# Performance work log

Hardware: AMD Instinct MI355X
Metric: run time of the kernel (lower is better)

Reference implementation:

```python
import jax, jax.numpy as jnp
import numpy as np

NT = 32          # nt_states
T = 64           # t_states
ST = NT + T      # total states
NEG = -1e9       # matches self.huge fill


def setup_inputs() -> dict:
    key = jax.random.key(0)
    k1, k2, k3 = jax.random.split(key, 3)
    B, n = 8, 28
    return {
        "unary_scores": jax.random.normal(k1, (B, n, T), dtype=jnp.float32),
        "rule_scores": jax.random.normal(k2, (B, NT, ST, ST), dtype=jnp.float32),
        "root_scores": jax.random.normal(k3, (B, NT), dtype=jnp.float32),
    }


def _inside(unary_scores, rule_scores, root_scores):
    # Chart indexed beta[b, width, start, state]; span (s, s+w) lives at [b, w, s].
    # Invalid (state-range) slots hold NEG, so exp() underflows them to exactly 0,
    # reproducing the terminal/nonterminal slice logic of the torch code.
    B, n, _ = unary_scores.shape
    beta = jnp.full((B, n, n, ST), NEG, dtype=unary_scores.dtype)
    beta = beta.at[:, 0, :, NT:].set(unary_scores)  # width-0 diagonal: preterminals

    mrule = rule_scores.max(axis=(2, 3))                    # [B, A]
    erule = jnp.exp(rule_scores - mrule[:, :, None, None])  # [B, A, L, R]

    for w in range(1, n):
        S = n - w                     # number of valid start positions
        k = np.arange(w)              # split offset: u = s + k
        # left child: span (s, s+k) -> width k, start s
        left = beta[:, :w, :S, :]                                  # [B, w, S, ST]
        # right child: span (s+k+1, s+w) -> width w-1-k, start s+k+1
        sr = k[:, None] + 1 + np.arange(S)[None, :]                # [w, S]
        right = beta[:, (w - 1 - k)[:, None], sr, :]               # [B, w, S, ST]

        # stable logsumexp over (k, l, r) via exp-space matmuls
        ml = left.max(-1)                                          # [B, w, S]
        mr = right.max(-1)                                         # [B, w, S]
        M = (ml + mr).max(1)                                       # [B, S]
        el = jnp.exp(left - ml[..., None])
        er = jnp.exp(right - mr[..., None] + (ml + mr - M[:, None, :])[..., None])
        numer = jnp.einsum('bksl,bksr->bslr', el, er)              # [B, S, L, R]
        total = jnp.einsum('bslr,balr->bsa', numer, erule)         # [B, S, A]
        score = jnp.log(total) + M[..., None] + mrule[:, None, :]
        beta = beta.at[:, w, :S, :NT].set(score)

    top = beta[:, n - 1, 0, :NT] + root_scores                     # span (0, n-1)
    return jax.nn.logsumexp(top, axis=1)                           # log Z, [B]


def reference(unary_scores, rule_scores, root_scores):
    return _inside(unary_scores, rule_scores, root_scores)
```

## Files before the change

kernel.cpp:

```cpp
#include <hip/hip_runtime.h>
#include <cstdint>
#include <cstddef>


#define NMAX 28
#define SLOT 17344
#define MROW 17280
#define MPROW 17312

#define O_BW1 0
#define O_BMX 960
#define O_G   1744
#define O_MSP 2528
#define O_EMR 2560
#define O_NUM 2592
#define O_RED 6160
#define O_ELT 20496
#define O_ELK 6160
#define O_ERK 14480
#define O_TRI 22800
#define LDSF  34864

__device__ __forceinline__ int off32(int w, int n) {
    return (w - 1) * n - (w * (w - 1)) / 2;
}
__device__ __forceinline__ float gload(const float* p) {
    return __hip_atomic_load(p, __ATOMIC_RELAXED, __HIP_MEMORY_SCOPE_AGENT);
}
__device__ __forceinline__ void gstore(float* p, float v) {
    __hip_atomic_store(p, v, __ATOMIC_RELAXED, __HIP_MEMORY_SCOPE_AGENT);
}
__device__ __forceinline__ unsigned gloadu(const unsigned* p) {
    return __hip_atomic_load(p, __ATOMIC_RELAXED, __HIP_MEMORY_SCOPE_AGENT);
}
__device__ __forceinline__ void gstoreu(unsigned* p, unsigned v) {
    __hip_atomic_store(p, v, __ATOMIC_RELAXED, __HIP_MEMORY_SCOPE_AGENT);
}
__device__ __forceinline__ float dot4acc(float4 m, float4 t, float acc) {
    return fmaf(m.x, t.x, fmaf(m.y, t.y, fmaf(m.z, t.z, fmaf(m.w, t.w, acc))));
}

__global__ __launch_bounds__(256) void mrule_kernel(const float* __restrict__ rule,
                                                    float* __restrict__ mrule,
                                                    unsigned* __restrict__ flags) {
    int a = blockIdx.x, b = blockIdx.y, tid = threadIdx.x;
    if (a == 0 && tid < 32)
        gstoreu(&flags[b * 32 + tid], (tid >= 16 && tid < 20) ? 2u : 0u);
    const float* base = rule + (size_t)(b * 32 + a) * 9216;
    float v = -3.0e38f;
    for (int i = tid; i < 9216; i += 256) v = fmaxf(v, base[i]);
    for (int off = 32; off > 0; off >>= 1) v = fmaxf(v, __shfl_xor(v, off, 64));
    __shared__ float red[4];
    if ((tid & 63) == 0) red[tid >> 6] = v;
    __syncthreads();
    if (tid == 0)
        mrule[b * 32 + a] = fmaxf(fmaxf(red[0], red[1]), fmaxf(red[2], red[3]));
}

__global__ __launch_bounds__(256) void pack_kernel(const float* __restrict__ rule,
                                                   const float* __restrict__ mrule,
                                                   float* __restrict__ E_TT,
                                                   float* __restrict__ E_TN,
                                                   float* __restrict__ E_NT,
                                                   float* __restrict__ E_NN) {
    int b = blockIdx.y, tid = threadIdx.x;
    int a = tid & 31;
    int cc = blockIdx.x * 8 + (tid >> 5);
    float mr = mrule[b * 32 + a];
    int l, r;
    float* dst;
    if (cc < 1024) {
        int flat = cc * 4;
        l = 32 + (flat >> 6); r = 32 + (flat & 63);
        dst = E_TT + ((size_t)(b * 1024 + cc) * 32 + a) * 4;
    } else if (cc < 1536) {
        int flat = (cc - 1024) * 4;
        l = 32 + (flat >> 5); r = flat & 31;
        dst = E_TN + ((size_t)(b * 512 + (cc - 1024)) * 32 + a) * 4;
    } else if (cc < 2048) {
        int flat = (cc - 1536) * 4;
        l = flat >> 6; r = 32 + (flat & 63);
        dst = E_NT + ((size_t)(b * 512 + (cc - 1536)) * 32 + a) * 4;
    } else {
        int flat = (cc - 2048) * 4;
        l = flat >> 5; r = flat & 31;
        dst = E_NN + ((size_t)(b * 256 + (cc - 2048)) * 32 + a) * 4;
    }
    const float4 v = *(const float4*)(rule + (((size_t)(b * 32 + a) * 96 + l) * 96 + r));
    float4 o;
    o.x = expf(v.x - mr); o.y = expf(v.y - mr);
    o.z = expf(v.z - mr); o.w = expf(v.w - mr);
    *(float4*)dst = o;
}

__device__ __forceinline__ void spin_flags(const unsigned* f, unsigned tgt, int tid) {
    if (tid < 64) {
        for (;;) {
            unsigned v = (tid < 20) ? gloadu(&f[tid]) : tgt;
            if (__ballot(v < tgt) == 0ull) break;
            __builtin_amdgcn_s_sleep(2);
        }
    }
    __syncthreads();
}

__global__ __launch_bounds__(1024, 4) void inside_kernel(
    const float* __restrict__ unary, const float* __restrict__ mrule,
    const float* __restrict__ E_TT, const float* __restrict__ E_TN,
    const float* __restrict__ E_NT, const float* __restrict__ E_NN,
    float* __restrict__ part, const float* __restrict__ root,
    float* __restrict__ out, unsigned* __restrict__ flags, int n) {
    extern __shared__ float lds[];
    const int b = blockIdx.x / 20, ch = blockIdx.x % 20;
    const int tid = threadIdx.x;
    const int a = tid & 31;
    unsigned* const myflags = flags + b * 32;
    float* const pbase = part + (size_t)(b * 4) * SLOT;

    float4 e4[2];
    {
        const float4* Eq;
        int base4;
        if (ch < 16) { Eq = (const float4*)E_TT + (size_t)b * 32768; base4 = ch * 64; }
        else         { Eq = (const float4*)E_NN + (size_t)b * 8192;  base4 = (ch - 16) * 64; }
        #pragma unroll
        for (int i = 0; i < 2; ++i)
            e4[i] = Eq[(size_t)(base4 + (tid >> 5) * 2 + i) * 32 + a];
    }
    if (tid < 32) lds[O_EMR + tid] = __expf(mrule[b * 32 + tid]);
    for (int pos = tid >> 6; pos < n; pos += 16) {
        int t = tid & 63;
        float v = unary[((size_t)b * n + pos) * 64 + t];
        float m = v;
        for (int off = 32; off > 0; off >>= 1) m = fmaxf(m, __shfl_xor(m, off, 64));
        if (t == 0) lds[O_BMX + pos] = m;
        if (ch < 16) lds[O_ELT + t * 29 + pos] = __expf(v - m);
    }
    __syncthreads();

    if (ch < 16) {
        for (int w = 1; w < n; ++w) {
            const int S = n - w;
            float* pbW = pbase + (size_t)(w & 3) * SLOT;

            if (w >= 2) {
                spin_flags(myflags, (unsigned)(w - 1), tid);
                const int wp = w - 1;
                const float* pbP = pbase + (size_t)(wp & 3) * SLOT;
                if (tid < (S + 1) * 32) {
                    int s = tid >> 5, aa = tid & 31;
                    float q[20];
                    #pragma unroll
                    for (int c = 0; c < 20; ++c) q[c] = gload(&pbP[c * 864 + tid]);
                    float tT = (((q[0] + q[1]) + (q[2] + q[3])) + ((q[4] + q[5]) + (q[6] + q[7])))
                             + (((q[8] + q[9]) + (q[10] + q[11])) + ((q[12] + q[13]) + (q[14] + q[15])));
                    float t = tT;
                    if (wp >= 3) {
                        float tN = (q[16] + q[17]) + (q[18] + q[19]);
                        float Mp = gload(&pbP[MPROW + s]);
                        t = fmaf(__expf(Mp - lds[O_MSP + s]), tN, tT);
                    }
                    float t2 = t * lds[O_EMR + aa];
                    float m2 = t2;
                    for (int off = 16; off > 0; off >>= 1)
                        m2 = fmaxf(m2, __shfl_xor(m2, off, 32));
                    lds[O_BW1 + aa * 30 + s] = t2 / m2;
                    if (aa == 0)
                        lds[O_BMX + wp * NMAX + s] = __logf(m2) + lds[O_MSP + s];
                }
                __syncthreads();
            }

            if (tid < S) {
                int s = tid;
                float M = -3.0e38f;
                for (int k = 0; k < w; ++k)
                    M = fmaxf(M, lds[O_BMX + k * NMAX + s] +
                                  lds[O_BMX + (w - 1 - k) * NMAX + s + k + 1]);
                lds[O_MSP + s] = M;
                lds[O_G + s] =
                    __expf(lds[O_BMX + s] + lds[O_BMX + (w - 1) * NMAX + s + 1] - M);
                lds[O_G + NMAX + s] =
                    __expf(lds[O_BMX + (w - 1) * NMAX + s] + lds[O_BMX + s + w] - M);
                if (ch == 0) gstore(&pbW[MROW + s], M);
            }
            __syncthreads();

            {
                const int cL = tid & 255, sh = tid >> 8;
                const bool tn = (w >= 2) && (ch < 8);
                const int cc = (w == 1) ? ch * 256 + cL
                             : (ch < 8 ? ch * 256 + cL : (ch - 8) * 256 + cL);
                int l, r;
                if (tn) { l = cc >> 5; r = cc & 31; }
                else    { l = cc >> 6; r = cc & 63; }
                unsigned short* np = (unsigned short*)(lds + O_NUM);
                for (int s = sh; s < S; s += 4) {
                    float v;
                    if (w == 1)
                        v = lds[O_ELT + l * 29 + s] * lds[O_ELT + r * 29 + (s + 1)] *
                            lds[O_G + s];
                    else if (tn)
                        v = lds[O_ELT + l * 29 + s] * lds[O_BW1 + r * 30 + (s + 1)] *
                            lds[O_G + s];
                    else
                        v = lds[O_BW1 + l * 30 + s] * lds[O_ELT + r * 29 + (s + w)] *
                            lds[O_G + NMAX + s];
                    unsigned u = __float_as_uint(v);
                    np[s * 264 + cL] = (unsigned short)((u + 0x7fffu + ((u >> 16) & 1u)) >> 16);
                }
            }
            __syncthreads();

            {
                const char* nbase = (const char*)(lds + O_NUM);
                const int g32 = tid >> 5, wv = tid >> 6;
                const bool lowhalf = (tid & 32) == 0;
                for (int s = 0; s < S; ++s) {
                    uint4 u = *(const uint4*)(nbase + s * 528 + g32 * 16);
                    float acc = 0.f;
                    #define LO(q) __uint_as_float((q) << 16)
                    #define HI(q) __uint_as_float((q) & 0xffff0000u)
                    acc = fmaf(LO(u.x), e4[0].x, acc); acc = fmaf(HI(u.x), e4[0].y, acc);
                    acc = fmaf(LO(u.y), e4[0].z, acc); acc = fmaf(HI(u.y), e4[0].w, acc);
                    acc = fmaf(LO(u.z), e4[1].x, acc); acc = fmaf(HI(u.z), e4[1].y, acc);
                    acc = fmaf(LO(u.w), e4[1].z, acc); acc = fmaf(HI(u.w), e4[1].w, acc);
                    #undef LO
                    #undef HI
                    acc += __shfl_xor(acc, 32, 64);
                    if (lowhalf) lds[O_RED + wv * 896 + s * 32 + a] = acc;
                }
            }
            __syncthreads();

            if (tid < S * 32) {
                float t = 0.f;
                #pragma unroll
                for (int g2 = 0; g2 < 16; ++g2) t += lds[O_RED + g2 * 896 + tid];
                gstore(&pbW[ch * 864 + tid], t);
            }
            __syncthreads();
            if (tid == 0) gstoreu(&myflags[ch], (unsigned)w);

            if (w == 1) {
                const float4* Eq = (ch < 8)
                    ? (const float4*)E_TN + (size_t)b * 16384 + (size_t)(ch * 64) * 32
                    : (const float4*)E_NT + (size_t)b * 16384 + (size_t)((ch - 8) * 64) * 32;
                #pragma unroll
                for (int i = 0; i < 2; ++i)
                    e4[i] = Eq[(size_t)((tid >> 5) * 2 + i) * 32 + a];
            }
        }

        if (ch == 0) {
            spin_flags(myflags, (unsigned)(n - 1), tid);
            if (tid < 32) {
                const float* pbP = pbase + (size_t)((n - 1) & 3) * SLOT;
                float q[20];
                #pragma unroll
                for (int c = 0; c < 20; ++c) q[c] = gload(&pbP[c * 864 + tid]);
                float tT = (((q[0] + q[1]) + (q[2] + q[3])) + ((q[4] + q[5]) + (q[6] + q[7])))
                         + (((q[8] + q[9]) + (q[10] + q[11])) + ((q[12] + q[13]) + (q[14] + q[15])));
                float tN = (q[16] + q[17]) + (q[18] + q[19]);
                float Mp = gload(&pbP[MPROW + 0]);
                float t = fmaf(__expf(Mp - lds[O_MSP + 0]), tN, tT);
                float v = __logf(t) + lds[O_MSP + 0] + mrule[b * 32 + tid] + root[b * 32 + tid];
                float m = v;
                for (int off = 16; off > 0; off >>= 1) m = fmaxf(m, __shfl_xor(m, off, 32));
                float e = __expf(v - m);
                for (int off = 16; off > 0; off >>= 1) e += __shfl_xor(e, off, 32);
                if (tid == 0) out[b] = m + __logf(e);
            }
        }
    } else {
        for (int w = 3; w < n; ++w) {
            const int S = n - w, Sp2 = S | 1;
            int q4 = (w - 2 + 3) >> 2; if (!(q4 & 1)) ++q4;
            const int K4 = 4 * q4;
            float* pbW = pbase + (size_t)(w & 3) * SLOT;

            spin_flags(myflags, (unsigned)(w - 2), tid);

            {
                const int wf = w - 2;
                const float* pbF = pbase + (size_t)(wf & 3) * SLOT;
                if (tid < (n - wf) * 32) {
                    int s = tid >> 5, aa = tid & 31;
                    float q[20];
                    #pragma unroll
                    for (int c = 0; c < 20; ++c) q[c] = gload(&pbF[c * 864 + tid]);
                    float tT = (((q[0] + q[1]) + (q[2] + q[3])) + ((q[4] + q[5]) + (q[6] + q[7])))
                             + (((q[8] + q[9]) + (q[10] + q[11])) + ((q[12] + q[13]) + (q[14] + q[15])));
                    float Mf = gload(&pbF[MROW + s]);
                    float t = tT;
                    if (wf >= 3) {
                        float tN = (q[16] + q[17]) + (q[18] + q[19]);
                        float Mp = gload(&pbF[MPROW + s]);
                        t = fmaf(__expf(Mp - Mf), tN, tT);
                    }
                    float t2 = t * lds[O_EMR + aa];
                    float m2 = t2;
                    for (int off = 16; off > 0; off >>= 1)
                        m2 = fmaxf(m2, __shfl_xor(m2, off, 32));
                    lds[O_TRI + (off32(wf, n) + s) * 32 + aa] = t2 / m2;
                    if (aa == 0) lds[O_BMX + wf * NMAX + s] = __logf(m2) + Mf;
                }
                __syncthreads();
            }

            if (tid < (w - 2) * 32) {
                int k = (tid >> 5) + 1, s = tid & 31;
                if (s < S) {
                    float Mp = -3.0e38f;
                    for (int k2 = 1; k2 <= w - 2; ++k2)
                        Mp = fmaxf(Mp, lds[O_BMX + k2 * NMAX + s] +
                                       lds[O_BMX + (w - 1 - k2) * NMAX + s + k2 + 1]);
                    lds[O_G + k * NMAX + s] =
                        __expf(lds[O_BMX + k * NMAX + s] +
                               lds[O_BMX + (w - 1 - k) * NMAX + s + k + 1] - Mp);
                    if (k == 1 && ch == 16) gstore(&pbW[MPROW + s], Mp);
                }
            }
            __syncthreads();

            if (tid < S * 32) {
                int s = tid >> 5, sym = tid & 31;
                int off = (sym * Sp2 + s) * K4;
                for (int kk = 1; kk <= w - 2; ++kk) {
                    lds[O_ELK + off + kk - 1] =
                        lds[O_TRI + (off32(kk, n) + s) * 32 + sym];
                    lds[O_ERK + off + kk - 1] =
                        lds[O_TRI + (off32(w - 1 - kk, n) + s + kk + 1) * 32 + sym] *
                        lds[O_G + kk * NMAX + s];
                }
                for (int k = w - 2; k < K4; ++k) {
                    lds[O_ELK + off + k] = 0.f;
                    lds[O_ERK + off + k] = 0.f;
                }
            }
            __syncthreads();

            {
                const int cL = tid & 255, sh = tid >> 8;
                const int cc = (ch - 16) * 256 + cL;
                const int l = cc >> 5, r = cc & 31;
                unsigned short* np = (unsigned short*)(lds + O_NUM);
                for (int s = sh; s < S; s += 4) {
                    const float* elp = lds + O_ELK + (l * Sp2 + s) * K4;
                    const float* erp = lds + O_ERK + (r * Sp2 + s) * K4;
                    float acc = 0.f;
                    for (int j = 0; j < K4; j += 4)
                        acc = dot4acc(*(const float4*)(elp + j),
                                      *(const float4*)(erp + j), acc);
                    unsigned u = __float_as_uint(acc);
                    np[s * 264 + cL] = (unsigned short)((u + 0x7fffu + ((u >> 16) & 1u)) >> 16);
                }
            }
            __syncthreads();

            {
                const char* nbase = (const char*)(lds + O_NUM);
                const int g32 = tid >> 5, wv = tid >> 6;
                const bool lowhalf = (tid & 32) == 0;
                for (int s = 0; s < S; ++s) {
                    uint4 u = *(const uint4*)(nbase + s * 528 + g32 * 16);
                    float acc = 0.f;
                    #define LO(q) __uint_as_float((q) << 16)
                    #define HI(q) __uint_as_float((q) & 0xffff0000u)
                    acc = fmaf(LO(u.x), e4[0].x, acc); acc = fmaf(HI(u.x), e4[0].y, acc);
                    acc = fmaf(LO(u.y), e4[0].z, acc); acc = fmaf(HI(u.y), e4[0].w, acc);
                    acc = fmaf(LO(u.z), e4[1].x, acc); acc = fmaf(HI(u.z), e4[1].y, acc);
                    acc = fmaf(LO(u.w), e4[1].z, acc); acc = fmaf(HI(u.w), e4[1].w, acc);
                    #undef LO
                    #undef HI
                    acc += __shfl_xor(acc, 32, 64);
                    if (lowhalf) lds[O_RED + wv * 896 + s * 32 + a] = acc;
                }
            }
            __syncthreads();

            if (tid < S * 32) {
                float t = 0.f;
                #pragma unroll
                for (int g2 = 0; g2 < 16; ++g2) t += lds[O_RED + g2 * 896 + tid];
                gstore(&pbW[ch * 864 + tid], t);
            }
            __syncthreads();
            if (tid == 0) gstoreu(&myflags[ch], (unsigned)w);
        }
    }
}

extern "C" void kernel_launch(void* const* d_in, const int* in_sizes, int n_in,
                              void* d_out, int out_size, void* d_ws, size_t ws_size,
                              hipStream_t stream) {
    const float* unary = (const float*)d_in[0];
    const float* rule  = (const float*)d_in[1];
    const float* root  = (const float*)d_in[2];
    float* out = (float*)d_out;

    const int B = in_sizes[2] / 32;
    int n = in_sizes[0] / (B * 64);

    float* ws = (float*)d_ws;
    float* mrule  = ws;
    float* E_TT   = mrule + (size_t)B * 32;
    float* E_TN   = E_TT + (size_t)B * 131072;
    float* E_NT   = E_TN + (size_t)B * 65536;
    float* E_NN   = E_NT + (size_t)B * 65536;
    float* part   = E_NN + (size_t)B * 32768;
    unsigned* flags = (unsigned*)(part + (size_t)B * 4 * SLOT);

    mrule_kernel<<<dim3(32, B), 256, 0, stream>>>(rule, mrule, flags);
    pack_kernel<<<dim3(288, B), 256, 0, stream>>>(rule, mrule, E_TT, E_TN, E_NT, E_NN);

    hipFuncSetAttribute((const void*)inside_kernel,
                        hipFuncAttributeMaxDynamicSharedMemorySize, LDSF * 4);

    void* args[] = {
        (void*)&unary, (void*)&mrule,
        (void*)&E_TT, (void*)&E_TN, (void*)&E_NT, (void*)&E_NN,
        (void*)&part, (void*)&root, (void*)&out, (void*)&flags, (void*)&n
    };
    hipLaunchCooperativeKernel((void*)inside_kernel, dim3(B * 20), dim3(1024),
                               args, LDSF * 4, stream);
}
```

Baseline: 242.7 us.

## Precontract terminal rule tensors with unary scores to shrink the inside recursion

```diff
diff --git a/kernel.cpp b/kernel.cpp
--- a/kernel.cpp
+++ b/kernel.cpp
@@ -4,22 +4,22 @@
 
 
 #define NMAX 28
-#define SLOT 17344
-#define MROW 17280
-#define MPROW 17312
-
-#define O_BW1 0
-#define O_BMX 960
-#define O_G   1744
-#define O_MSP 2528
-#define O_EMR 2560
-#define O_NUM 2592
-#define O_RED 6160
-#define O_ELT 20496
-#define O_ELK 6160
-#define O_ERK 14480
-#define O_TRI 22800
-#define LDSF  34864
+#define SLOTF 10368
+#define T_ELT 0
+#define T_BW1 1856
+#define T_BMX 2816
+#define T_MSP 3600
+#define T_GG  3632
+#define T_HB  3712
+#define T_FB  10880
+#define N_BMX 0
+#define N_GP  784
+#define N_NUM 1568
+#define N_RED 5132
+#define N_ELK 5132
+#define N_ERK 13452
+#define N_TRI 21772
+#define LDSF  33836
 
 __device__ __forceinline__ int off32(int w, int n) {
     return (w - 1) * n - (w * (w - 1)) / 2;
@@ -39,185 +39,306 @@
 __device__ __forceinline__ float dot4acc(float4 m, float4 t, float acc) {
     return fmaf(m.x, t.x, fmaf(m.y, t.y, fmaf(m.z, t.z, fmaf(m.w, t.w, acc))));
 }
-
-__global__ __launch_bounds__(256) void mrule_kernel(const float* __restrict__ rule,
-                                                    float* __restrict__ mrule,
-                                                    unsigned* __restrict__ flags) {
-    int a = blockIdx.x, b = blockIdx.y, tid = threadIdx.x;
-    if (a == 0 && tid < 32)
-        gstoreu(&flags[b * 32 + tid], (tid >= 16 && tid < 20) ? 2u : 0u);
-    const float* base = rule + (size_t)(b * 32 + a) * 9216;
-    float v = -3.0e38f;
-    for (int i = tid; i < 9216; i += 256) v = fmaxf(v, base[i]);
-    for (int off = 32; off > 0; off >>= 1) v = fmaxf(v, __shfl_xor(v, off, 64));
-    __shared__ float red[4];
-    if ((tid & 63) == 0) red[tid >> 6] = v;
-    __syncthreads();
-    if (tid == 0)
-        mrule[b * 32 + a] = fmaxf(fmaxf(red[0], red[1]), fmaxf(red[2], red[3]));
-}
-
-__global__ __launch_bounds__(256) void pack_kernel(const float* __restrict__ rule,
-                                                   const float* __restrict__ mrule,
-                                                   float* __restrict__ E_TT,
-                                                   float* __restrict__ E_TN,
-                                                   float* __restrict__ E_NT,
-                                                   float* __restrict__ E_NN) {
-    int b = blockIdx.y, tid = threadIdx.x;
-    int a = tid & 31;
-    int cc = blockIdx.x * 8 + (tid >> 5);
-    float mr = mrule[b * 32 + a];
-    int l, r;
-    float* dst;
-    if (cc < 1024) {
-        int flat = cc * 4;
-        l = 32 + (flat >> 6); r = 32 + (flat & 63);
-        dst = E_TT + ((size_t)(b * 1024 + cc) * 32 + a) * 4;
-    } else if (cc < 1536) {
-        int flat = (cc - 1024) * 4;
-        l = 32 + (flat >> 5); r = flat & 31;
-        dst = E_TN + ((size_t)(b * 512 + (cc - 1024)) * 32 + a) * 4;
-    } else if (cc < 2048) {
-        int flat = (cc - 1536) * 4;
-        l = flat >> 6; r = 32 + (flat & 63);
-        dst = E_NT + ((size_t)(b * 512 + (cc - 1536)) * 32 + a) * 4;
-    } else {
-        int flat = (cc - 2048) * 4;
-        l = flat >> 5; r = flat & 31;
-        dst = E_NN + ((size_t)(b * 256 + (cc - 2048)) * 32 + a) * 4;
-    }
-    const float4 v = *(const float4*)(rule + (((size_t)(b * 32 + a) * 96 + l) * 96 + r));
-    float4 o;
-    o.x = expf(v.x - mr); o.y = expf(v.y - mr);
-    o.z = expf(v.z - mr); o.w = expf(v.w - mr);
-    *(float4*)dst = o;
-}
-
-__device__ __forceinline__ void spin_flags(const unsigned* f, unsigned tgt, int tid) {
+__device__ __forceinline__ float maxM(const float* bmx, int w, int s) {
+    float M = -3.0e38f;
+    for (int k = 0; k < w; ++k)
+        M = fmaxf(M, bmx[k * NMAX + s] + bmx[(w - 1 - k) * NMAX + s + k + 1]);
+    return M;
+}
+__device__ __forceinline__ float maxMp(const float* bmx, int w, int s) {
+    float M = -3.0e38f;
+    for (int k = 1; k <= w - 2; ++k)
+        M = fmaxf(M, bmx[k * NMAX + s] + bmx[(w - 1 - k) * NMAX + s + k + 1]);
+    return M;
+}
+__device__ __forceinline__ float finalize_sum(const float* pp, bool hasNN,
+                                              float Mp, float Mw) {
+    float x[12];
+    #pragma unroll
+    for (int c = 0; c < 12; ++c) x[c] = gload(pp + c);
+    float tT = (((x[0] + x[1]) + (x[2] + x[3])) + ((x[4] + x[5]) + (x[6] + x[7])));
+    float t = tT;
+    if (hasNN) {
+        float tN = (x[8] + x[9]) + (x[10] + x[11]);
+        t = fmaf(__expf(Mp - Mw), tN, tT);
+    }
+    return t;
+}
+__device__ __forceinline__ void spin12(const unsigned* f, unsigned tgt, int tid) {
     if (tid < 64) {
         for (;;) {
-            unsigned v = (tid < 20) ? gloadu(&f[tid]) : tgt;
+            unsigned v = (tid < 12) ? gloadu(&f[tid]) : tgt;
             if (__ballot(v < tgt) == 0ull) break;
-            __builtin_amdgcn_s_sleep(2);
+            __builtin_amdgcn_s_sleep(1);
         }
     }
     __syncthreads();
 }
 
-__global__ __launch_bounds__(1024, 4) void inside_kernel(
-    const float* __restrict__ unary, const float* __restrict__ mrule,
-    const float* __restrict__ E_TT, const float* __restrict__ E_TN,
-    const float* __restrict__ E_NT, const float* __restrict__ E_NN,
+__global__ __launch_bounds__(256) void prep_kernel(const float* __restrict__ unary,
+                                                   float* __restrict__ elT_g,
+                                                   float* __restrict__ bmax0_g,
+                                                   unsigned* __restrict__ flags, int n) {
+    int b = blockIdx.x, tid = threadIdx.x;
+    if (tid < 12) gstoreu(&flags[b * 32 + tid], (tid >= 8) ? 2u : 0u);
+    for (int pos = tid >> 6; pos < n; pos += 4) {
+        int t = tid & 63;
+        float v = unary[((size_t)(b * n) + pos) * 64 + t];
+        float m = v;
+        for (int off = 32; off > 0; off >>= 1) m = fmaxf(m, __shfl_xor(m, off, 64));
+        elT_g[(size_t)b * 64 * n + t * n + pos] = __expf(v - m);
+        if (t == 0) bmax0_g[b * 32 + pos] = m;
+    }
+}
+
+__global__ __launch_bounds__(256) void pack_kernel(const float* __restrict__ rule,
+                                                   const float* __restrict__ elT_g,
+                                                   float* __restrict__ H_g,
+                                                   float* __restrict__ F_g,
+                                                   float* __restrict__ G_g,
+                                                   float* __restrict__ E_NN, int n) {
+    extern __shared__ float sl[];
+    int b = blockIdx.y, aa = blockIdx.x, tid = threadIdx.x;
+    const float4* rs4 = (const float4*)(rule + (size_t)(b * 32 + aa) * 9216);
+    for (int i = tid; i < 2304; i += 256) {
+        float4 v = rs4[i];
+        float4 o;
+        o.x = __expf(v.x); o.y = __expf(v.y); o.z = __expf(v.z); o.w = __expf(v.w);
+        ((float4*)sl)[i] = o;
+    }
+    for (int i = tid; i < 64 * n; i += 256)
+        sl[9216 + i] = elT_g[(size_t)b * 64 * n + i];
+    __syncthreads();
+    const float* elt = sl + 9216;
+    {
+        int c4 = tid;
+        if (c4 < 256) {
+            int flat = c4 * 4, l = flat >> 5, r = flat & 31;
+            float4 o = *(const float4*)(sl + l * 96 + r);
+            *(float4*)(E_NN + ((size_t)(b * 256 + c4) * 32 + aa) * 4) = o;
+        }
+    }
+    for (int i = tid; i < 64 * n; i += 256) {
+        int r = i / n, s = i - r * n;
+        float acc = 0.f;
+        for (int l = 0; l < 64; ++l)
+            acc = fmaf(elt[l * n + s], sl[(32 + l) * 96 + 32 + r], acc);
+        H_g[((size_t)(b * 64 + r) * n + s) * 32 + aa] = acc;
+    }
+    for (int i = tid; i < 32 * n; i += 256) {
+        int r = i / n, s = i - r * n;
+        float acc = 0.f;
+        for (int l = 0; l < 64; ++l)
+            acc = fmaf(elt[l * n + s], sl[(32 + l) * 96 + r], acc);
+        F_g[((size_t)(b * 32 + r) * n + s) * 32 + aa] = acc;
+    }
+    for (int i = tid; i < 32 * n; i += 256) {
+        int l = i / n, s = i - l * n;
+        float acc = 0.f;
+        for (int r = 0; r < 64; ++r)
+            acc = fmaf(elt[r * n + s], sl[l * 96 + 32 + r], acc);
+        G_g[((size_t)(b * 32 + l) * n + s) * 32 + aa] = acc;
+    }
+}
+
+__global__ __launch_bounds__(1024, 1) void inside_kernel(
+    const float* __restrict__ elT_g, const float* __restrict__ bmax0_g,
+    const float* __restrict__ H_g, const float* __restrict__ F_g,
+    const float* __restrict__ G_g, const float* __restrict__ E_NN,
     float* __restrict__ part, const float* __restrict__ root,
     float* __restrict__ out, unsigned* __restrict__ flags, int n) {
     extern __shared__ float lds[];
-    const int b = blockIdx.x / 20, ch = blockIdx.x % 20;
+    const int b = blockIdx.x / 12, ch = blockIdx.x % 12;
     const int tid = threadIdx.x;
     const int a = tid & 31;
     unsigned* const myflags = flags + b * 32;
-    float* const pbase = part + (size_t)(b * 4) * SLOT;
-
-    float4 e4[2];
-    {
-        const float4* Eq;
-        int base4;
-        if (ch < 16) { Eq = (const float4*)E_TT + (size_t)b * 32768; base4 = ch * 64; }
-        else         { Eq = (const float4*)E_NN + (size_t)b * 8192;  base4 = (ch - 16) * 64; }
-        #pragma unroll
-        for (int i = 0; i < 2; ++i)
-            e4[i] = Eq[(size_t)(base4 + (tid >> 5) * 2 + i) * 32 + a];
-    }
-    if (tid < 32) lds[O_EMR + tid] = __expf(mrule[b * 32 + tid]);
-    for (int pos = tid >> 6; pos < n; pos += 16) {
-        int t = tid & 63;
-        float v = unary[((size_t)b * n + pos) * 64 + t];
-        float m = v;
-        for (int off = 32; off > 0; off >>= 1) m = fmaxf(m, __shfl_xor(m, off, 64));
-        if (t == 0) lds[O_BMX + pos] = m;
-        if (ch < 16) lds[O_ELT + t * 29 + pos] = __expf(v - m);
-    }
-    __syncthreads();
-
-    if (ch < 16) {
+    float* const pbase = part + (size_t)(b * 4) * SLOTF;
+
+    if (ch < 8) {
+        for (int i = tid; i < 64 * n; i += 1024) {
+            int t = i / n, pos = i - t * n;
+            lds[T_ELT + t * 29 + pos] = elT_g[(size_t)b * 64 * n + i];
+        }
+        for (int i = tid; i < 8 * n * 32; i += 1024)
+            lds[T_HB + i] = H_g[(size_t)(b * 64 + ch * 8) * n * 32 + i];
+        {
+            const float* src = (ch < 4)
+                ? F_g + (size_t)(b * 32 + ch * 8) * n * 32
+                : G_g + (size_t)(b * 32 + (ch - 4) * 8) * n * 32;
+            for (int i = tid; i < 8 * n * 32; i += 1024) lds[T_FB + i] = src[i];
+        }
+        if (tid < n) lds[T_BMX + tid] = bmax0_g[b * 32 + tid];
+        __syncthreads();
+
         for (int w = 1; w < n; ++w) {
             const int S = n - w;
-            float* pbW = pbase + (size_t)(w & 3) * SLOT;
+            float* pbW = pbase + (size_t)(w & 3) * SLOTF;
 
             if (w >= 2) {
-                spin_flags(myflags, (unsigned)(w - 1), tid);
+                spin12(myflags, (unsigned)(w - 1), tid);
                 const int wp = w - 1;
-                const float* pbP = pbase + (size_t)(wp & 3) * SLOT;
+                const bool hasNN = (wp >= 3);
+                const float* pbP = pbase + (size_t)(wp & 3) * SLOTF;
                 if (tid < (S + 1) * 32) {
                     int s = tid >> 5, aa = tid & 31;
-                    float q[20];
-                    #pragma unroll
-                    for (int c = 0; c < 20; ++c) q[c] = gload(&pbP[c * 864 + tid]);
-                    float tT = (((q[0] + q[1]) + (q[2] + q[3])) + ((q[4] + q[5]) + (q[6] + q[7])))
-                             + (((q[8] + q[9]) + (q[10] + q[11])) + ((q[12] + q[13]) + (q[14] + q[15])));
-                    float t = tT;
-                    if (wp >= 3) {
-                        float tN = (q[16] + q[17]) + (q[18] + q[19]);
-                        float Mp = gload(&pbP[MPROW + s]);
-                        t = fmaf(__expf(Mp - lds[O_MSP + s]), tN, tT);
-                    }
-                    float t2 = t * lds[O_EMR + aa];
-                    float m2 = t2;
+                    float Mp = maxMp(lds + T_BMX, wp, s);
+                    float t = finalize_sum(pbP + (size_t)tid * 12, hasNN,
+                                           Mp, lds[T_MSP + s]);
+                    float m2 = t;
                     for (int off = 16; off > 0; off >>= 1)
                         m2 = fmaxf(m2, __shfl_xor(m2, off, 32));
-                    lds[O_BW1 + aa * 30 + s] = t2 / m2;
+                    lds[T_BW1 + aa * 30 + s] = t / m2;
                     if (aa == 0)
-                        lds[O_BMX + wp * NMAX + s] = __logf(m2) + lds[O_MSP + s];
+                        lds[T_BMX + wp * NMAX + s] = __logf(m2) + lds[T_MSP + s];
                 }
                 __syncthreads();
             }
 
             if (tid < S) {
                 int s = tid;
-                float M = -3.0e38f;
-                for (int k = 0; k < w; ++k)
-                    M = fmaxf(M, lds[O_BMX + k * NMAX + s] +
-                                  lds[O_BMX + (w - 1 - k) * NMAX + s + k + 1]);
-                lds[O_MSP + s] = M;
-                lds[O_G + s] =
-                    __expf(lds[O_BMX + s] + lds[O_BMX + (w - 1) * NMAX + s + 1] - M);
-                lds[O_G + NMAX + s] =
-                    __expf(lds[O_BMX + (w - 1) * NMAX + s] + lds[O_BMX + s + w] - M);
-                if (ch == 0) gstore(&pbW[MROW + s], M);
+                float M = maxM(lds + T_BMX, w, s);
+                lds[T_MSP + s] = M;
+                lds[T_GG + s] =
+                    __expf(lds[T_BMX + s] + lds[T_BMX + (w - 1) * NMAX + s + 1] - M);
+                lds[T_GG + 32 + s] =
+                    __expf(lds[T_BMX + (w - 1) * NMAX + s] + lds[T_BMX + s + w] - M);
+            }
+            __syncthreads();
+
+            if (tid < S * 32) {
+                int s = tid >> 5;
+                float acc = 0.f;
+                if (w == 1) {
+                    #pragma unroll
+                    for (int j = 0; j < 8; ++j)
+                        acc = fmaf(lds[T_ELT + (ch * 8 + j) * 29 + (s + 1)],
+                                   lds[T_HB + (j * n + s) * 32 + a], acc);
+                } else if (ch < 4) {
+                    #pragma unroll
+                    for (int j = 0; j < 8; ++j)
+                        acc = fmaf(lds[T_BW1 + (ch * 8 + j) * 30 + (s + 1)],
+                                   lds[T_FB + (j * n + s) * 32 + a], acc);
+                    acc *= lds[T_GG + s];
+                } else {
+                    #pragma unroll
+                    for (int j = 0; j < 8; ++j)
+                        acc = fmaf(lds[T_BW1 + ((ch - 4) * 8 + j) * 30 + s],
+                                   lds[T_FB + (j * n + (s + w)) * 32 + a], acc);
+                    acc *= lds[T_GG + 32 + s];
+                }
+                gstore(&pbW[(size_t)tid * 12 + ch], acc);
+            }
+            __syncthreads();
+            if (tid == 0) gstoreu(&myflags[ch], (unsigned)w);
+        }
+
+        if (ch == 0) {
+            spin12(myflags, (unsigned)(n - 1), tid);
+            if (tid < 32) {
+                const int wp = n - 1;
+                const float* pbP = pbase + (size_t)(wp & 3) * SLOTF;
+                float Mp = maxMp(lds + T_BMX, wp, 0);
+                float t = finalize_sum(pbP + (size_t)tid * 12, true,
+                                       Mp, lds[T_MSP + 0]);
+                float v = __logf(t) + lds[T_MSP + 0] + root[b * 32 + tid];
+                float m = v;
+                for (int off = 16; off > 0; off >>= 1)
+                    m = fmaxf(m, __shfl_xor(m, off, 32));
+                float e = __expf(v - m);
+                for (int off = 16; off > 0; off >>= 1) e += __shfl_xor(e, off, 32);
+                if (tid == 0) out[b] = m + __logf(e);
+            }
+        }
+    } else {
+        float4 e4[2];
+        {
+            const float4* Eq = (const float4*)E_NN + (size_t)b * 8192;
+            int base = (ch - 8) * 64 + (tid >> 5) * 2;
+            e4[0] = Eq[(size_t)base * 32 + a];
+            e4[1] = Eq[(size_t)(base + 1) * 32 + a];
+        }
+        if (tid < n) lds[N_BMX + tid] = bmax0_g[b * 32 + tid];
+        __syncthreads();
+
+        for (int w = 3; w < n; ++w) {
+            const int S = n - w, Sp2 = S | 1;
+            int q4 = (w - 2 + 3) >> 2; if (!(q4 & 1)) ++q4;
+            const int K4 = 4 * q4;
+            float* pbW = pbase + (size_t)(w & 3) * SLOTF;
+
+            spin12(myflags, (unsigned)(w - 2), tid);
+
+            {
+                const int wf = w - 2;
+                const bool hasNN = (wf >= 3);
+                const float* pbF_ = pbase + (size_t)(wf & 3) * SLOTF;
+                if (tid < (n - wf) * 32) {
+                    int s = tid >> 5, aa = tid & 31;
+                    float Mw = maxM(lds + N_BMX, wf, s);
+                    float Mp = maxMp(lds + N_BMX, wf, s);
+                    float t = finalize_sum(pbF_ + (size_t)tid * 12, hasNN, Mp, Mw);
+                    float m2 = t;
+                    for (int off = 16; off > 0; off >>= 1)
+                        m2 = fmaxf(m2, __shfl_xor(m2, off, 32));
+                    lds[N_TRI + (off32(wf, n) + s) * 32 + aa] = t / m2;
+                    if (aa == 0) lds[N_BMX + wf * NMAX + s] = __logf(m2) + Mw;
+                }
+                __syncthreads();
+            }
+
+            if (tid < (w - 2) * 32) {
+                int k = (tid >> 5) + 1, s = tid & 31;
+                if (s < S) {
+                    float Mp = maxMp(lds + N_BMX, w, s);
+                    lds[N_GP + k * NMAX + s] =
+                        __expf(lds[N_BMX + k * NMAX + s] +
+                               lds[N_BMX + (w - 1 - k) * NMAX + s + k + 1] - Mp);
+                }
+            }
+            __syncthreads();
+
+            if (tid < S * 32) {
+                int s = tid >> 5, sym = tid & 31;
+                int off = (sym * Sp2 + s) * K4;
+                for (int kk = 1; kk <= w - 2; ++kk) {
+                    lds[N_ELK + off + kk - 1] =
+                        lds[N_TRI + (off32(kk, n) + s) * 32 + sym];
+                    lds[N_ERK + off + kk - 1] =
+                        lds[N_TRI + (off32(w - 1 - kk, n) + s + kk + 1) * 32 + sym] *
+                        lds[N_GP + kk * NMAX + s];
+                }
+                for (int k = w - 2; k < K4; ++k) {
+                    lds[N_ELK + off + k] = 0.f;
+                    lds[N_ERK + off + k] = 0.f;
+                }
             }
             __syncthreads();
 
             {
                 const int cL = tid & 255, sh = tid >> 8;
-                const bool tn = (w >= 2) && (ch < 8);
-                const int cc = (w == 1) ? ch * 256 + cL
-                             : (ch < 8 ? ch * 256 + cL : (ch - 8) * 256 + cL);
-                int l, r;
-                if (tn) { l = cc >> 5; r = cc & 31; }
-                else    { l = cc >> 6; r = cc & 63; }
-                unsigned short* np = (unsigned short*)(lds + O_NUM);
+                const int cc = (ch - 8) * 256 + cL;
+                const int l = cc >> 5, r = cc & 31;
+                unsigned short* np = (unsigned short*)(lds + N_NUM);
                 for (int s = sh; s < S; s += 4) {
-                    float v;
-                    if (w == 1)
-                        v = lds[O_ELT + l * 29 + s] * lds[O_ELT + r * 29 + (s + 1)] *
-                            lds[O_G + s];
-                    else if (tn)
-                        v = lds[O_ELT + l * 29 + s] * lds[O_BW1 + r * 30 + (s + 1)] *
-                            lds[O_G + s];
-                    else
-                        v = lds[O_BW1 + l * 30 + s] * lds[O_ELT + r * 29 + (s + w)] *
-                            lds[O_G + NMAX + s];
-                    unsigned u = __float_as_uint(v);
-                    np[s * 264 + cL] = (unsigned short)((u + 0x7fffu + ((u >> 16) & 1u)) >> 16);
+                    const float* elp = lds + N_ELK + (l * Sp2 + s) * K4;
+                    const float* erp = lds + N_ERK + (r * Sp2 + s) * K4;
+                    float acc = 0.f;
+                    for (int j = 0; j < K4; j += 4)
+                        acc = dot4acc(*(const float4*)(elp + j),
+                                      *(const float4*)(erp + j), acc);
+                    unsigned u = __float_as_uint(acc);
+                    np[s * 264 + cL] =
+                        (unsigned short)((u + 0x7fffu + ((u >> 16) & 1u)) >> 16);
                 }
             }
             __syncthreads();
 
             {
-                const char* nbase = (const char*)(lds + O_NUM);
-                const int g32 = tid >> 5, wv = tid >> 6;
-                const bool lowhalf = (tid & 32) == 0;
+                const char* nb = (const char*)(lds + N_NUM);
+                const int g = tid >> 5, wv = tid >> 6;
+                const bool low = (tid & 32) == 0;
                 for (int s = 0; s < S; ++s) {
-                    uint4 u = *(const uint4*)(nbase + s * 528 + g32 * 16);
+                    uint4 u = *(const uint4*)(nb + s * 528 + g * 16);
                     float acc = 0.f;
                     #define LO(q) __uint_as_float((q) << 16)
                     #define HI(q) __uint_as_float((q) & 0xffff0000u)
@@ -228,7 +349,7 @@
                     #undef LO
                     #undef HI
                     acc += __shfl_xor(acc, 32, 64);
-                    if (lowhalf) lds[O_RED + wv * 896 + s * 32 + a] = acc;
+                    if (low) lds[N_RED + wv * 896 + s * 32 + a] = acc;
                 }
             }
             __syncthreads();
@@ -236,154 +357,8 @@
             if (tid < S * 32) {
                 float t = 0.f;
                 #pragma unroll
-                for (int g2 = 0; g2 < 16; ++g2) t += lds[O_RED + g2 * 896 + tid];
-                gstore(&pbW[ch * 864 + tid], t);
-            }
-            __syncthreads();
-            if (tid == 0) gstoreu(&myflags[ch], (unsigned)w);
-
-            if (w == 1) {
-                const float4* Eq = (ch < 8)
-                    ? (const float4*)E_TN + (size_t)b * 16384 + (size_t)(ch * 64) * 32
-                    : (const float4*)E_NT + (size_t)b * 16384 + (size_t)((ch - 8) * 64) * 32;
-                #pragma unroll
-                for (int i = 0; i < 2; ++i)
-                    e4[i] = Eq[(size_t)((tid >> 5) * 2 + i) * 32 + a];
-            }
-        }
-
-        if (ch == 0) {
-            spin_flags(myflags, (unsigned)(n - 1), tid);
-            if (tid < 32) {
-                const float* pbP = pbase + (size_t)((n - 1) & 3) * SLOT;
-                float q[20];
-                #pragma unroll
-                for (int c = 0; c < 20; ++c) q[c] = gload(&pbP[c * 864 + tid]);
-                float tT = (((q[0] + q[1]) + (q[2] + q[3])) + ((q[4] + q[5]) + (q[6] + q[7])))
-                         + (((q[8] + q[9]) + (q[10] + q[11])) + ((q[12] + q[13]) + (q[14] + q[15])));
-                float tN = (q[16] + q[17]) + (q[18] + q[19]);
-                float Mp = gload(&pbP[MPROW + 0]);
-                float t = fmaf(__expf(Mp - lds[O_MSP + 0]), tN, tT);
-                float v = __logf(t) + lds[O_MSP + 0] + mrule[b * 32 + tid] + root[b * 32 + tid];
-                float m = v;
-                for (int off = 16; off > 0; off >>= 1) m = fmaxf(m, __shfl_xor(m, off, 32));
-                float e = __expf(v - m);
-                for (int off = 16; off > 0; off >>= 1) e += __shfl_xor(e, off, 32);
-                if (tid == 0) out[b] = m + __logf(e);
-            }
-        }
-    } else {
-        for (int w = 3; w < n; ++w) {
-            const int S = n - w, Sp2 = S | 1;
-            int q4 = (w - 2 + 3) >> 2; if (!(q4 & 1)) ++q4;
-            const int K4 = 4 * q4;
-            float* pbW = pbase + (size_t)(w & 3) * SLOT;
-
-            spin_flags(myflags, (unsigned)(w - 2), tid);
-
-            {
-                const int wf = w - 2;
-                const float* pbF = pbase + (size_t)(wf & 3) * SLOT;
-                if (tid < (n - wf) * 32) {
-                    int s = tid >> 5, aa = tid & 31;
-                    float q[20];
-                    #pragma unroll
-                    for (int c = 0; c < 20; ++c) q[c] = gload(&pbF[c * 864 + tid]);
-                    float tT = (((q[0] + q[1]) + (q[2] + q[3])) + ((q[4] + q[5]) + (q[6] + q[7])))
-                             + (((q[8] + q[9]) + (q[10] + q[11])) + ((q[12] + q[13]) + (q[14] + q[15])));
-                    float Mf = gload(&pbF[MROW + s]);
-                    float t = tT;
-                    if (wf >= 3) {
-                        float tN = (q[16] + q[17]) + (q[18] + q[19]);
-                        float Mp = gload(&pbF[MPROW + s]);
-                        t = fmaf(__expf(Mp - Mf), tN, tT);
-                    }
-                    float t2 = t * lds[O_EMR + aa];
-                    float m2 = t2;
-                    for (int off = 16; off > 0; off >>= 1)
-                        m2 = fmaxf(m2, __shfl_xor(m2, off, 32));
-                    lds[O_TRI + (off32(wf, n) + s) * 32 + aa] = t2 / m2;
-                    if (aa == 0) lds[O_BMX + wf * NMAX + s] = __logf(m2) + Mf;
-                }
-                __syncthreads();
-            }
-
-            if (tid < (w - 2) * 32) {
-                int k = (tid >> 5) + 1, s = tid & 31;
-                if (s < S) {
-                    float Mp = -3.0e38f;
-                    for (int k2 = 1; k2 <= w - 2; ++k2)
-                        Mp = fmaxf(Mp, lds[O_BMX + k2 * NMAX + s] +
-                                       lds[O_BMX + (w - 1 - k2) * NMAX + s + k2 + 1]);
-                    lds[O_G + k * NMAX + s] =
-                        __expf(lds[O_BMX + k * NMAX + s] +
-                               lds[O_BMX + (w - 1 - k) * NMAX + s + k + 1] - Mp);
-                    if (k == 1 && ch == 16) gstore(&pbW[MPROW + s], Mp);
-                }
-            }
-            __syncthreads();
-
-            if (tid < S * 32) {
-                int s = tid >> 5, sym = tid & 31;
-                int off = (sym * Sp2 + s) * K4;
-                for (int kk = 1; kk <= w - 2; ++kk) {
-                    lds[O_ELK + off + kk - 1] =
-                        lds[O_TRI + (off32(kk, n) + s) * 32 + sym];
-                    lds[O_ERK + off + kk - 1] =
-                        lds[O_TRI + (off32(w - 1 - kk, n) + s + kk + 1) * 32 + sym] *
-                        lds[O_G + kk * NMAX + s];
-                }
-                for (int k = w - 2; k < K4; ++k) {
-                    lds[O_ELK + off + k] = 0.f;
-                    lds[O_ERK + off + k] = 0.f;
-                }
-            }
-            __syncthreads();
-
-            {
-                const int cL = tid & 255, sh = tid >> 8;
-                const int cc = (ch - 16) * 256 + cL;
-                const int l = cc >> 5, r = cc & 31;
-                unsigned short* np = (unsigned short*)(lds + O_NUM);
-                for (int s = sh; s < S; s += 4) {
-                    const float* elp = lds + O_ELK + (l * Sp2 + s) * K4;
-                    const float* erp = lds + O_ERK + (r * Sp2 + s) * K4;
-                    float acc = 0.f;
-                    for (int j = 0; j < K4; j += 4)
-                        acc = dot4acc(*(const float4*)(elp + j),
-                                      *(const float4*)(erp + j), acc);
-                    unsigned u = __float_as_uint(acc);
-                    np[s * 264 + cL] = (unsigned short)((u + 0x7fffu + ((u >> 16) & 1u)) >> 16);
-                }
-            }
-            __syncthreads();
-
-            {
-                const char* nbase = (const char*)(lds + O_NUM);
-                const int g32 = tid >> 5, wv = tid >> 6;
-                const bool lowhalf = (tid & 32) == 0;
-                for (int s = 0; s < S; ++s) {
-                    uint4 u = *(const uint4*)(nbase + s * 528 + g32 * 16);
-                    float acc = 0.f;
-                    #define LO(q) __uint_as_float((q) << 16)
-                    #define HI(q) __uint_as_float((q) & 0xffff0000u)
-                    acc = fmaf(LO(u.x), e4[0].x, acc); acc = fmaf(HI(u.x), e4[0].y, acc);
-                    acc = fmaf(LO(u.y), e4[0].z, acc); acc = fmaf(HI(u.y), e4[0].w, acc);
-                    acc = fmaf(LO(u.z), e4[1].x, acc); acc = fmaf(HI(u.z), e4[1].y, acc);
-                    acc = fmaf(LO(u.w), e4[1].z, acc); acc = fmaf(HI(u.w), e4[1].w, acc);
-                    #undef LO
-                    #undef HI
-                    acc += __shfl_xor(acc, 32, 64);
-                    if (lowhalf) lds[O_RED + wv * 896 + s * 32 + a] = acc;
-                }
-            }
-            __syncthreads();
-
-            if (tid < S * 32) {
-                float t = 0.f;
-                #pragma unroll
-                for (int g2 = 0; g2 < 16; ++g2) t += lds[O_RED + g2 * 896 + tid];
-                gstore(&pbW[ch * 864 + tid], t);
+                for (int g2 = 0; g2 < 16; ++g2) t += lds[N_RED + g2 * 896 + tid];
+                gstore(&pbW[(size_t)tid * 12 + ch], t);
             }
             __syncthreads();
             if (tid == 0) gstoreu(&myflags[ch], (unsigned)w);
@@ -403,25 +378,30 @@
     int n = in_sizes[0] / (B * 64);
 
     float* ws = (float*)d_ws;
-    float* mrule  = ws;
-    float* E_TT   = mrule + (size_t)B * 32;
-    float* E_TN   = E_TT + (size_t)B * 131072;
-    float* E_NT   = E_TN + (size_t)B * 65536;
-    float* E_NN   = E_NT + (size_t)B * 65536;
-    float* part   = E_NN + (size_t)B * 32768;
-    unsigned* flags = (unsigned*)(part + (size_t)B * 4 * SLOT);
-
-    mrule_kernel<<<dim3(32, B), 256, 0, stream>>>(rule, mrule, flags);
-    pack_kernel<<<dim3(288, B), 256, 0, stream>>>(rule, mrule, E_TT, E_TN, E_NT, E_NN);
+    float* elT_g = ws;
+    float* bmax0 = elT_g + (size_t)B * 64 * n;
+    float* H_g   = bmax0 + (size_t)B * 32;
+    float* F_g   = H_g + (size_t)B * 64 * n * 32;
+    float* G_g   = F_g + (size_t)B * 32 * n * 32;
+    float* E_NN  = G_g + (size_t)B * 32 * n * 32;
+    float* part  = E_NN + (size_t)B * 32768;
+    unsigned* flags = (unsigned*)(part + (size_t)B * 4 * SLOTF);
+
+    prep_kernel<<<dim3(B), 256, 0, stream>>>(unary, elT_g, bmax0, flags, n);
+
+    const int packLds = (9216 + 64 * n) * 4;
+    hipFuncSetAttribute((const void*)pack_kernel,
+                        hipFuncAttributeMaxDynamicSharedMemorySize, packLds);
+    pack_kernel<<<dim3(32, B), 256, packLds, stream>>>(rule, elT_g, H_g, F_g,
+                                                       G_g, E_NN, n);
 
     hipFuncSetAttribute((const void*)inside_kernel,
                         hipFuncAttributeMaxDynamicSharedMemorySize, LDSF * 4);
-
     void* args[] = {
-        (void*)&unary, (void*)&mrule,
-        (void*)&E_TT, (void*)&E_TN, (void*)&E_NT, (void*)&E_NN,
-        (void*)&part, (void*)&root, (void*)&out, (void*)&flags, (void*)&n
+        (void*)&elT_g, (void*)&bmax0, (void*)&H_g, (void*)&F_g, (void*)&G_g,
+        (void*)&E_NN, (void*)&part, (void*)&root, (void*)&out,
+        (void*)&flags, (void*)&n
     };
-    hipLaunchCooperativeKernel((void*)inside_kernel, dim3(B * 20), dim3(1024),
+    hipLaunchCooperativeKernel((void*)inside_kernel, dim3(B * 12), dim3(1024),
                                args, LDSF * 4, stream);
 }
```

Result: slower. 315.1 us (+29.8%).
